# Optimization experiments

Hardware: AMD Instinct MI355X
Metric: run time of the kernel (lower is better)

Reference implementation:

```python
import jax, jax.numpy as jnp
import numpy as np

N = 8192      # num_nodes
E = 262144    # edges (before self loops)
F_IN = 256    # input_dim
H = 4         # nheads
C = 32        # nhid (per-head out channels)
D = H * C     # concat dim = 128
NEG_SLOPE = 0.2
EPS = 1e-5


def setup_inputs() -> dict:
    key = jax.random.key(0)
    ks = jax.random.split(key, 12)
    s = 0.05
    x = jax.random.normal(ks[0], (N, F_IN), jnp.float32)
    adj = jax.random.randint(ks[1], (2, E), 0, N, dtype=jnp.int32)
    Wgat = jax.random.normal(ks[2], (F_IN, D), jnp.float32) * s   # GATConv lin weight
    att_src = jax.random.normal(ks[3], (H, C), jnp.float32) * s
    att_dst = jax.random.normal(ks[4], (H, C), jnp.float32) * s
    bias_gat = jax.random.normal(ks[5], (D,), jnp.float32) * s
    Wq = jax.random.normal(ks[6], (H, D, C), jnp.float32) * s     # per-head selfattention query proj
    Wk = jax.random.normal(ks[7], (H, D, C), jnp.float32) * s     # per-head selfattention key proj
    Wpro = jax.random.normal(ks[8], (D, D), jnp.float32) * s      # prolayer (no bias)
    ln_g = jnp.ones((D,), jnp.float32)
    ln_b = jnp.zeros((D,), jnp.float32)
    return {"x": x, "adj": adj, "Wgat": Wgat, "att_src": att_src,
            "att_dst": att_dst, "bias_gat": bias_gat, "Wq": Wq, "Wk": Wk,
            "Wpro": Wpro, "ln_g": ln_g, "ln_b": ln_b}


def _gat_conv(x, src, dst, Wgat, att_src, att_dst, bias_gat):
    # PyG GATConv, concat=True, add_self_loops handled by caller.
    xw = (x @ Wgat).reshape(N, H, C)                       # [N,H,C]
    a_src = jnp.einsum('nhc,hc->nh', xw, att_src)          # [N,H]
    a_dst = jnp.einsum('nhc,hc->nh', xw, att_dst)
    e = jax.nn.leaky_relu(a_src[src] + a_dst[dst], NEG_SLOPE)  # [Etot,H]
    # segment softmax over incoming edges of each destination node
    m = jax.ops.segment_max(e, dst, num_segments=N)        # [N,H]
    e = jnp.exp(e - m[dst])
    denom = jax.ops.segment_sum(e, dst, num_segments=N)    # [N,H]
    alpha = e / denom[dst]                                 # [Etot,H]
    out = jax.ops.segment_sum(xw[src] * alpha[:, :, None], dst, num_segments=N)
    return out.reshape(N, D) + bias_gat                    # [N,D]


def reference(x, adj, Wgat, att_src, att_dst, bias_gat, Wq, Wk, Wpro, ln_g, ln_b):
    # add self loops (PyG GATConv default)
    loops = jnp.arange(N, dtype=adj.dtype)
    src = jnp.concatenate([adj[0], loops])
    dst = jnp.concatenate([adj[1], loops])

    h_cat = _gat_conv(x, src, dst, Wgat, att_src, att_dst, bias_gat)  # [N,D]
    h = h_cat @ Wpro                                                   # prolayer

    # sum over nheads independent dense node self-attention heads
    q = jnp.einsum('nd,hdc->hnc', h, Wq)                   # [H,N,C]
    k = jnp.einsum('nd,hdc->hnc', h, Wk)
    scores = jnp.einsum('hnc,hmc->hnm', q, k) / jnp.sqrt(jnp.float32(C))  # [H,N,N]
    att = jax.nn.softmax(scores, axis=-1)
    temp = jnp.einsum('hnm,md->nd', att, h)                # sum of per-head att @ h

    y = temp + h                                           # residual
    mu = jnp.mean(y, axis=-1, keepdims=True)
    var = jnp.mean(jnp.square(y - mu), axis=-1, keepdims=True)
    return (y - mu) / jnp.sqrt(var + EPS) * ln_g + ln_b
```

## Files before the change

kernel.cpp:

```cpp
#include <hip/hip_runtime.h>
#include <math.h>

#define N_NODES 8192
#define E_EDGES 262144
#define ETOT (E_EDGES + N_NODES)
#define F_IN 256
#define NH 4
#define NC 32
#define DD 128
#define NEG_SLOPE 0.2f
#define LN_EPS 1e-5f
#define QK_SCALE (1.4426950408889634f / 5.656854249492381f)

typedef __attribute__((ext_vector_type(8))) short bf16x8;
typedef __attribute__((ext_vector_type(4))) float f32x4;

__device__ __forceinline__ float fexp2(float x) { return __builtin_amdgcn_exp2f(x); }
__device__ __forceinline__ float flog2(float x) { return __builtin_amdgcn_logf(x); }
__device__ __forceinline__ float frcp(float x)  { return __builtin_amdgcn_rcpf(x); }

__device__ __forceinline__ unsigned short f2bf(float f) {
    unsigned u = __float_as_uint(f);
    u += 0x7FFFu + ((u >> 16) & 1u);
    return (unsigned short)(u >> 16);
}
__device__ __forceinline__ unsigned pk2bf(float lo, float hi) {
    unsigned a = __float_as_uint(lo) + 0x8000u;
    unsigned b = __float_as_uint(hi) + 0x8000u;
    return __builtin_amdgcn_perm(b, a, 0x07060302u);
}

__global__ __launch_bounds__(256) void k_cvt(const float* __restrict__ Wgat,
                                             const float* __restrict__ Wpro,
                                             const float* __restrict__ Wq,
                                             const float* __restrict__ Wk,
                                             unsigned short* __restrict__ Wgt,
                                             unsigned short* __restrict__ Wpt,
                                             unsigned short* __restrict__ Wqt,
                                             unsigned short* __restrict__ Wkt) {
    int t = blockIdx.x * 256 + threadIdx.x;
    if (t < 32768) {
        int c = t >> 8, k = t & 255;
        Wgt[t] = f2bf(Wgat[(size_t)k * 128 + c]);
    } else if (t < 49152) {
        int i = t - 32768, c = i >> 7, k = i & 127;
        Wpt[i] = f2bf(Wpro[(size_t)k * 128 + c]);
    } else if (t < 65536) {
        int i = t - 49152, h = i >> 12, r = i & 4095, c = r >> 7, k = r & 127;
        Wqt[i] = f2bf(Wq[h * 4096 + k * 32 + c]);
    } else if (t < 81920) {
        int i = t - 65536, h = i >> 12, r = i & 4095, c = r >> 7, k = r & 127;
        Wkt[i] = f2bf(Wk[h * 4096 + k * 32 + c]);
    }
}

__global__ __launch_bounds__(256) void k_gemm_att(const float* __restrict__ x,
                                                  const unsigned short* __restrict__ Wgt,
                                                  const float* __restrict__ att_src,
                                                  const float* __restrict__ att_dst,
                                                  float* __restrict__ xw,
                                                  float* __restrict__ asrc,
                                                  float* __restrict__ adst) {
    __shared__ unsigned short xs[32 * 256];
    const int tid = threadIdx.x;
    const int w = tid >> 6, lane = tid & 63, lq = lane & 15, g = lane >> 4;
    const int n0 = blockIdx.x * 32;
#pragma unroll
    for (int m = 0; m < 4; ++m) {
        int lin = m * 256 + tid;
        int row = lin >> 5, ch = lin & 31;
        const float* src = &x[(size_t)(n0 + row) * 256 + ch * 8];
        float4 v0 = *(const float4*)src;
        float4 v1 = *(const float4*)(src + 4);
        uint4 o;
        o.x = (unsigned)f2bf(v0.x) | ((unsigned)f2bf(v0.y) << 16);
        o.y = (unsigned)f2bf(v0.z) | ((unsigned)f2bf(v0.w) << 16);
        o.z = (unsigned)f2bf(v1.x) | ((unsigned)f2bf(v1.y) << 16);
        o.w = (unsigned)f2bf(v1.z) | ((unsigned)f2bf(v1.w) << 16);
        *(uint4*)&xs[row * 256 + ((ch + row) & 31) * 8] = o;
    }
    __syncthreads();
    f32x4 zero = {0.f, 0.f, 0.f, 0.f};
    f32x4 acc[2][2];
#pragma unroll
    for (int s = 0; s < 2; ++s) { acc[s][0] = zero; acc[s][1] = zero; }
#pragma unroll
    for (int kb = 0; kb < 8; ++kb) {
        bf16x8 af[2], bf[2];
#pragma unroll
        for (int s = 0; s < 2; ++s) {
            int row = s * 16 + lq;
            af[s] = *(const bf16x8*)&xs[row * 256 + (((kb * 4 + g) + row) & 31) * 8];
        }
#pragma unroll
        for (int c = 0; c < 2; ++c)
            bf[c] = *(const bf16x8*)(Wgt + (size_t)(w * 32 + c * 16 + lq) * 256 + kb * 32 + g * 8);
#pragma unroll
        for (int s = 0; s < 2; ++s)
#pragma unroll
            for (int c = 0; c < 2; ++c)
                acc[s][c] = __builtin_amdgcn_mfma_f32_16x16x32_bf16(af[s], bf[c], acc[s][c], 0, 0, 0);
    }
#pragma unroll
    for (int s = 0; s < 2; ++s)
#pragma unroll
        for (int c = 0; c < 2; ++c)
#pragma unroll
            for (int r = 0; r < 4; ++r)
                xw[(size_t)(n0 + s * 16 + 4 * g + r) * DD + w * 32 + c * 16 + lq] = acc[s][c][r];
    float avs0 = att_src[w * 32 + lq],      avd0 = att_dst[w * 32 + lq];
    float avs1 = att_src[w * 32 + 16 + lq], avd1 = att_dst[w * 32 + 16 + lq];
#pragma unroll
    for (int s = 0; s < 2; ++s) {
        f32x4 vs, vd;
#pragma unroll
        for (int r = 0; r < 4; ++r) {
            vs[r] = acc[s][0][r] * avs0 + acc[s][1][r] * avs1;
            vd[r] = acc[s][0][r] * avd0 + acc[s][1][r] * avd1;
        }
#pragma unroll
        for (int off = 1; off < 16; off <<= 1)
#pragma unroll
            for (int r = 0; r < 4; ++r) {
                vs[r] += __shfl_xor(vs[r], off);
                vd[r] += __shfl_xor(vd[r], off);
            }
        if (lq == 0) {
#pragma unroll
            for (int r = 0; r < 4; ++r) {
                asrc[(n0 + s * 16 + 4 * g + r) * 4 + w] = vs[r];
                adst[(n0 + s * 16 + 4 * g + r) * 4 + w] = vd[r];
            }
        }
    }
}

__global__ __launch_bounds__(256) void k_gemm_pro(const float* __restrict__ hcat,
                                                  const unsigned short* __restrict__ Wpt,
                                                  const unsigned short* __restrict__ Wqt,
                                                  const unsigned short* __restrict__ Wkt,
                                                  float* __restrict__ hbuf,
                                                  unsigned short* __restrict__ Htb,
                                                  unsigned short* __restrict__ Qb,
                                                  unsigned short* __restrict__ Kb) {
    __shared__ unsigned short xs[32 * 128];
    __shared__ unsigned short hsd[32 * 128];
    const int tid = threadIdx.x;
    const int w = tid >> 6, lane = tid & 63, lq = lane & 15, g = lane >> 4;
    const int n0 = blockIdx.x * 32;
#pragma unroll
    for (int m = 0; m < 2; ++m) {
        int lin = m * 256 + tid;
        int row = lin >> 4, ch = lin & 15;
        const float* src = &hcat[(size_t)(n0 + row) * 128 + ch * 8];
        float4 v0 = *(const float4*)src;
        float4 v1 = *(const float4*)(src + 4);
        uint4 o;
        o.x = (unsigned)f2bf(v0.x) | ((unsigned)f2bf(v0.y) << 16);
        o.y = (unsigned)f2bf(v0.z) | ((unsigned)f2bf(v0.w) << 16);
        o.z = (unsigned)f2bf(v1.x) | ((unsigned)f2bf(v1.y) << 16);
        o.w = (unsigned)f2bf(v1.z) | ((unsigned)f2bf(v1.w) << 16);
        *(uint4*)&xs[row * 128 + ((ch + row) & 15) * 8] = o;
    }
    __syncthreads();
    f32x4 zero = {0.f, 0.f, 0.f, 0.f};
    f32x4 acc[2][2];
#pragma unroll
    for (int s = 0; s < 2; ++s) { acc[s][0] = zero; acc[s][1] = zero; }
#pragma unroll
    for (int kb = 0; kb < 4; ++kb) {
        bf16x8 af[2], bf[2];
#pragma unroll
        for (int s = 0; s < 2; ++s) {
            int row = s * 16 + lq;
            af[s] = *(const bf16x8*)&xs[row * 128 + (((kb * 4 + g) + row) & 15) * 8];
        }
#pragma unroll
        for (int c = 0; c < 2; ++c)
            bf[c] = *(const bf16x8*)(Wpt + (size_t)(w * 32 + c * 16 + lq) * 128 + kb * 32 + g * 8);
#pragma unroll
        for (int s = 0; s < 2; ++s)
#pragma unroll
            for (int c = 0; c < 2; ++c)
                acc[s][c] = __builtin_amdgcn_mfma_f32_16x16x32_bf16(af[s], bf[c], acc[s][c], 0, 0, 0);
    }
#pragma unroll
    for (int s = 0; s < 2; ++s)
#pragma unroll
        for (int c = 0; c < 2; ++c) {
            int col = w * 32 + c * 16 + lq;
#pragma unroll
            for (int r = 0; r < 4; ++r) {
                int row = s * 16 + 4 * g + r;
                hbuf[(size_t)(n0 + row) * 128 + col] = acc[s][c][r];
                hsd[row * 128 + (((col >> 3) + row) & 15) * 8 + (col & 7)] = f2bf(acc[s][c][r]);
            }
            uint2 hp;
            hp.x = pk2bf(acc[s][c][0], acc[s][c][1]);
            hp.y = pk2bf(acc[s][c][2], acc[s][c][3]);
            *(uint2*)(Htb + (size_t)col * N_NODES + n0 + s * 16 + 4 * g) = hp;
        }
    __syncthreads();
    f32x4 aq[2][2], ak[2][2];
#pragma unroll
    for (int s = 0; s < 2; ++s)
#pragma unroll
        for (int c = 0; c < 2; ++c) { aq[s][c] = zero; ak[s][c] = zero; }
#pragma unroll
    for (int kb = 0; kb < 4; ++kb) {
        bf16x8 af[2], bq[2], bk[2];
#pragma unroll
        for (int s = 0; s < 2; ++s) {
            int row = s * 16 + lq;
            af[s] = *(const bf16x8*)&hsd[row * 128 + (((kb * 4 + g) + row) & 15) * 8];
        }
#pragma unroll
        for (int c = 0; c < 2; ++c) {
            size_t widx = ((size_t)w * 32 + c * 16 + lq) * 128 + kb * 32 + g * 8;
            bq[c] = *(const bf16x8*)(Wqt + widx);
            bk[c] = *(const bf16x8*)(Wkt + widx);
        }
#pragma unroll
        for (int s = 0; s < 2; ++s)
#pragma unroll
            for (int c = 0; c < 2; ++c) {
                aq[s][c] = __builtin_amdgcn_mfma_f32_16x16x32_bf16(af[s], bq[c], aq[s][c], 0, 0, 0);
                ak[s][c] = __builtin_amdgcn_mfma_f32_16x16x32_bf16(af[s], bk[c], ak[s][c], 0, 0, 0);
            }
    }
#pragma unroll
    for (int s = 0; s < 2; ++s)
#pragma unroll
        for (int c = 0; c < 2; ++c)
#pragma unroll
            for (int r = 0; r < 4; ++r) {
                size_t nidx = (size_t)w * N_NODES + n0 + s * 16 + 4 * g + r;
                Qb[nidx * NC + c * 16 + lq] = f2bf(aq[s][c][r] * QK_SCALE);
                Kb[nidx * NC + c * 16 + lq] = f2bf(ak[s][c][r]);
            }
}

__device__ __forceinline__ void edge_sd(int e, const int* adj, int& s, int& d) {
    if (e < E_EDGES) { s = adj[e]; d = adj[E_EDGES + e]; }
    else { s = e - E_EDGES; d = s; }
}

__global__ void k_deg(const int* __restrict__ adj, int* __restrict__ deg) {
    int e = blockIdx.x * blockDim.x + threadIdx.x;
    if (e >= ETOT) return;
    int d = (e < E_EDGES) ? adj[E_EDGES + e] : e - E_EDGES;
    atomicAdd(&deg[d], 1);
}

__global__ __launch_bounds__(1024) void k_scan(const int* __restrict__ deg,
                                               int* __restrict__ rowptr,
                                               int* __restrict__ cursor) {
    __shared__ int sm[1024];
    int t = threadIdx.x;
    int v[8], sum = 0;
#pragma unroll
    for (int j = 0; j < 8; ++j) { v[j] = deg[t * 8 + j]; sum += v[j]; }
    sm[t] = sum;
    __syncthreads();
    for (int off = 1; off < 1024; off <<= 1) {
        int x = (t >= off) ? sm[t - off] : 0;
        __syncthreads();
        sm[t] += x;
        __syncthreads();
    }
    int base = sm[t] - sum;
#pragma unroll
    for (int j = 0; j < 8; ++j) {
        rowptr[t * 8 + j] = base;
        cursor[t * 8 + j] = base;
        base += v[j];
    }
    if (t == 1023) rowptr[8192] = base;
}

__global__ void k_fill(const int* __restrict__ adj, const float* __restrict__ asrc,
                       const float* __restrict__ adst, int* __restrict__ cursor,
                       int* __restrict__ src_csr, float* __restrict__ p_csr,
                       float* __restrict__ nodesum) {
    int e = blockIdx.x * blockDim.x + threadIdx.x;
    if (e >= ETOT) return;
    int s, d; edge_sd(e, adj, s, d);
    int pos = atomicAdd(&cursor[d], 1);
    float4 as4 = *(const float4*)&asrc[s * 4];
    float4 ad4 = *(const float4*)&adst[d * 4];
    const float L2E = 1.4426950408889634f;
    float v;
    float4 p;
    v = as4.x + ad4.x; v = v > 0.f ? v : NEG_SLOPE * v; p.x = fexp2(v * L2E);
    v = as4.y + ad4.y; v = v > 0.f ? v : NEG_SLOPE * v; p.y = fexp2(v * L2E);
    v = as4.z + ad4.z; v = v > 0.f ? v : NEG_SLOPE * v; p.z = fexp2(v * L2E);
    v = as4.w + ad4.w; v = v > 0.f ? v : NEG_SLOPE * v; p.w = fexp2(v * L2E);
    src_csr[pos] = s;
    *(float4*)&p_csr[(size_t)pos * 4] = p;
    atomicAdd(&nodesum[d * 4 + 0], p.x);
    atomicAdd(&nodesum[d * 4 + 1], p.y);
    atomicAdd(&nodesum[d * 4 + 2], p.z);
    atomicAdd(&nodesum[d * 4 + 3], p.w);
}

__global__ __launch_bounds__(256) void k_aggregate(const int* __restrict__ rowptr,
                                                   const int* __restrict__ src_csr,
                                                   const float* __restrict__ p_csr,
                                                   const float* __restrict__ nodesum,
                                                   const float* __restrict__ xw,
                                                   const float* __restrict__ bias,
                                                   float* __restrict__ hcat) {
    int n = blockIdx.x * 2 + (threadIdx.x >> 7);
    int c = threadIdx.x & 127;
    int h = c >> 5;
    int beg = rowptr[n], end = rowptr[n + 1];
    float rden = frcp(nodesum[n * 4 + h]);
    float acc = bias[c];
    int i = beg;
    for (; i + 4 <= end; i += 4) {
        int s0 = src_csr[i], s1 = src_csr[i + 1], s2 = src_csr[i + 2], s3 = src_csr[i + 3];
        float a0 = p_csr[(size_t)i * 4 + h];
        float a1 = p_csr[(size_t)(i + 1) * 4 + h];
        float a2 = p_csr[(size_t)(i + 2) * 4 + h];
        float a3 = p_csr[(size_t)(i + 3) * 4 + h];
        acc += a0 * xw[(size_t)s0 * DD + c] + a1 * xw[(size_t)s1 * DD + c]
             + a2 * xw[(size_t)s2 * DD + c] + a3 * xw[(size_t)s3 * DD + c];
    }
    for (; i < end; ++i) {
        int s0 = src_csr[i];
        acc += p_csr[(size_t)i * 4 + h] * xw[(size_t)s0 * DD + c];
    }
    float norm = acc - bias[c];
    hcat[(size_t)n * DD + c] = bias[c] + norm * rden;
}

__global__ __launch_bounds__(256) void k_attn_l(const unsigned short* __restrict__ Qb,
                                                const unsigned short* __restrict__ Kb,
                                                float* __restrict__ lsum) {
    const int tid = threadIdx.x;
    const int w = tid >> 6;
    const int lane = tid & 63;
    const int lq = lane & 15;
    const int g = lane >> 4;
    const int q0 = blockIdx.x * 64;
    const int ks = blockIdx.y;
    f32x4 zero = {0.f, 0.f, 0.f, 0.f};

    bf16x8 qf[4];
#pragma unroll
    for (int j = 0; j < 4; ++j)
        qf[j] = *(const bf16x8*)(Qb + ((size_t)w * N_NODES + q0 + j * 16 + lq) * NC + g * 8);
    const unsigned short* Kp = Kb + (size_t)w * N_NODES * NC;

    float l[4] = {0.f, 0.f, 0.f, 0.f};
    for (int kt = 0; kt < 16; ++kt) {
        const int k0 = ks * 1024 + kt * 64;
#pragma unroll
        for (int t = 0; t < 4; ++t) {
            const bf16x8 kf = *(const bf16x8*)(Kp + (size_t)(k0 + t * 16 + lq) * NC + g * 8);
#pragma unroll
            for (int j = 0; j < 4; ++j) {
                f32x4 st = __builtin_amdgcn_mfma_f32_16x16x32_bf16(kf, qf[j], zero, 0, 0, 0);
                l[j] += (fexp2(st[0]) + fexp2(st[1])) + (fexp2(st[2]) + fexp2(st[3]));
            }
        }
    }
#pragma unroll
    for (int j = 0; j < 4; ++j) {
        float lj = l[j];
        lj += __shfl_xor(lj, 16); lj += __shfl_xor(lj, 32);
        if (lane < 16) atomicAdd(&lsum[w * N_NODES + q0 + j * 16 + lq], lj);
    }
}

__global__ __launch_bounds__(256, 2) void k_attn_pv(
        const unsigned short* __restrict__ Qb,
        const unsigned short* __restrict__ Kb,
        const unsigned short* __restrict__ Htb,
        const float* __restrict__ lsum,
        float* __restrict__ Opart) {
    __shared__ unsigned short htl[128 * 64];
    __shared__ unsigned short plds[32 * 64];
    const int tid = threadIdx.x;
    const int w = tid >> 6;
    const int lane = tid & 63;
    const int lq = lane & 15;
    const int g = lane >> 4;
    const int q0 = blockIdx.x * 32;
    const int ks = blockIdx.y;
    const int sd = tid >> 3, sc = tid & 7;
    f32x4 zero = {0.f, 0.f, 0.f, 0.f};

    float lg0[4], lg1[4];
    bf16x8 qreg0[4], qreg1[4];
#pragma unroll
    for (int h = 0; h < 4; ++h) {
        lg0[h] = -flog2(lsum[h * N_NODES + q0 + lq]);
        lg1[h] = -flog2(lsum[h * N_NODES + q0 + 16 + lq]);
        qreg0[h] = *(const bf16x8*)(Qb + ((size_t)h * N_NODES + q0 + lq) * NC + g * 8);
        qreg1[h] = *(const bf16x8*)(Qb + ((size_t)h * N_NODES + q0 + 16 + lq) * NC + g * 8);
    }

    f32x4 acc[2][2];
#pragma unroll
    for (int a = 0; a < 2; ++a) { acc[a][0] = zero; acc[a][1] = zero; }

    const int wch = 2 * w + (g >> 1);
    const int whalf = (g & 1) * 8;

    for (int kt = 0; kt < 16; ++kt) {
        const int k0 = ks * 1024 + kt * 64;
        __syncthreads();
#pragma unroll
        for (int mm = 0; mm < 4; ++mm) {
            int d = mm * 32 + sd;
            uint4 v = *(const uint4*)(Htb + (size_t)d * N_NODES + k0 + sc * 8);
            *(uint4*)&htl[d * 64 + ((sc + d) & 7) * 8] = v;
        }
        f32x4 ps0 = zero, ps1 = zero;
#pragma unroll
        for (int h = 0; h < 4; ++h) {
            const bf16x8 kf = *(const bf16x8*)(Kb + ((size_t)h * N_NODES + k0 + w * 16 + lq) * NC + g * 8);
            f32x4 st0 = __builtin_amdgcn_mfma_f32_16x16x32_bf16(kf, qreg0[h], zero, 0, 0, 0);
            f32x4 st1 = __builtin_amdgcn_mfma_f32_16x16x32_bf16(kf, qreg1[h], zero, 0, 0, 0);
#pragma unroll
            for (int r = 0; r < 4; ++r) {
                ps0[r] += fexp2(st0[r] + lg0[h]);
                ps1[r] += fexp2(st1[r] + lg1[h]);
            }
        }
        uint2 pk;
        pk.x = pk2bf(ps0[0], ps0[1]); pk.y = pk2bf(ps0[2], ps0[3]);
        {
            int row = lq;
            *(uint2*)((char*)plds + row * 128 + ((wch + row) & 7) * 16 + whalf) = pk;
        }
        pk.x = pk2bf(ps1[0], ps1[1]); pk.y = pk2bf(ps1[2], ps1[3]);
        {
            int row = 16 + lq;
            *(uint2*)((char*)plds + row * 128 + ((wch + row) & 7) * 16 + whalf) = pk;
        }
        __syncthreads();
#pragma unroll
        for (int kc = 0; kc < 2; ++kc) {
            int row0 = lq, row1 = 16 + lq;
            const bf16x8 af0 = *(const bf16x8*)((char*)plds + row0 * 128 + ((kc * 4 + g + row0) & 7) * 16);
            const bf16x8 af1 = *(const bf16x8*)((char*)plds + row1 * 128 + ((kc * 4 + g + row1) & 7) * 16);
#pragma unroll
            for (int dl = 0; dl < 2; ++dl) {
                int dd = (w * 2 + dl) * 16 + lq;
                const bf16x8 bf = *(const bf16x8*)&htl[dd * 64 + ((kc * 4 + g + dd) & 7) * 8];
                acc[dl][0] = __builtin_amdgcn_mfma_f32_16x16x32_bf16(af0, bf, acc[dl][0], 0, 0, 0);
                acc[dl][1] = __builtin_amdgcn_mfma_f32_16x16x32_bf16(af1, bf, acc[dl][1], 0, 0, 0);
            }
        }
    }
    const size_t ob = (size_t)ks * N_NODES + q0;
#pragma unroll
    for (int dl = 0; dl < 2; ++dl) {
        int d = (w * 2 + dl) * 16 + lq;
#pragma unroll
        for (int s = 0; s < 2; ++s)
#pragma unroll
            for (int r = 0; r < 4; ++r)
                Opart[(ob + s * 16 + 4 * g + r) * DD + d] = acc[dl][s][r];
    }
}

__global__ __launch_bounds__(128) void k_finalize(const float* __restrict__ Opart,
                                                  const float* __restrict__ hb,
                                                  const float* __restrict__ g,
                                                  const float* __restrict__ b,
                                                  float* __restrict__ out) {
    __shared__ float red[2];
    int n = blockIdx.x, c = threadIdx.x;
    const size_t ND = (size_t)N_NODES * DD;
    size_t idx = (size_t)n * DD + c;
    float y = hb[idx];
#pragma unroll
    for (int i = 0; i < 8; ++i) y += Opart[i * ND + idx];
    float s = y;
#pragma unroll
    for (int off = 1; off < 64; off <<= 1) s += __shfl_xor(s, off);
    if ((c & 63) == 0) red[c >> 6] = s;
    __syncthreads();
    float mu = (red[0] + red[1]) * (1.f / 128.f);
    float dv = y - mu;
    float vs = dv * dv;
#pragma unroll
    for (int off = 1; off < 64; off <<= 1) vs += __shfl_xor(vs, off);
    __syncthreads();
    if ((c & 63) == 0) red[c >> 6] = vs;
    __syncthreads();
    float rstd = rsqrtf((red[0] + red[1]) * (1.f / 128.f) + LN_EPS);
    out[idx] = dv * rstd * g[c] + b[c];
}

extern "C" void kernel_launch(void* const* d_in, const int* in_sizes, int n_in,
                              void* d_out, int out_size, void* d_ws, size_t ws_size,
                              hipStream_t stream) {
    const float* x        = (const float*)d_in[0];
    const int*   adj      = (const int*)d_in[1];
    const float* Wgat     = (const float*)d_in[2];
    const float* att_src  = (const float*)d_in[3];
    const float* att_dst  = (const float*)d_in[4];
    const float* bias_gat = (const float*)d_in[5];
    const float* Wq       = (const float*)d_in[6];
    const float* Wk       = (const float*)d_in[7];
    const float* Wpro     = (const float*)d_in[8];
    const float* ln_g     = (const float*)d_in[9];
    const float* ln_b     = (const float*)d_in[10];
    float* out = (float*)d_out;

    const size_t ND = (size_t)N_NODES * DD;
    unsigned short* Qb  = (unsigned short*)d_ws;
    unsigned short* Kb  = Qb + (1 << 20);
    unsigned short* Htb = Kb + (1 << 20);
    unsigned short* Wgt = Htb + (1 << 20);
    unsigned short* Wpt = Wgt + 32768;
    unsigned short* Wqt = Wpt + 16384;
    unsigned short* Wkt = Wqt + 16384;
    float* xw      = (float*)(Wkt + 16384);
    float* hcat    = xw + ND;
    float* hbuf    = hcat + ND;
    float* asrc    = hbuf + ND;
    float* adst    = asrc + N_NODES * NH;
    float* nodesum = adst + N_NODES * NH;
    float* lsum    = nodesum + N_NODES * NH;
    int*   deg     = (int*)(lsum + N_NODES * NH);
    int*   rowptr  = deg + 8192;
    int*   cursor  = rowptr + 8704;
    int*   src_csr = cursor + 8704;
    float* p_csr   = (float*)(src_csr + ETOT);
    float* Opart   = p_csr + (size_t)ETOT * 4;

    hipMemsetAsync(nodesum, 0, 2 * N_NODES * NH * sizeof(float), stream);
    hipMemsetAsync(deg, 0, N_NODES * sizeof(int), stream);
    k_cvt<<<320, 256, 0, stream>>>(Wgat, Wpro, Wq, Wk, Wgt, Wpt, Wqt, Wkt);
    k_gemm_att<<<N_NODES / 32, 256, 0, stream>>>(x, Wgt, att_src, att_dst, xw, asrc, adst);
    int eblocks = (ETOT + 255) / 256;
    k_deg<<<eblocks, 256, 0, stream>>>(adj, deg);
    k_scan<<<1, 1024, 0, stream>>>(deg, rowptr, cursor);
    k_fill<<<eblocks, 256, 0, stream>>>(adj, asrc, adst, cursor, src_csr, p_csr, nodesum);
    k_aggregate<<<N_NODES / 2, 256, 0, stream>>>(rowptr, src_csr, p_csr, nodesum, xw, bias_gat, hcat);
    k_gemm_pro<<<N_NODES / 32, 256, 0, stream>>>(hcat, Wpt, Wqt, Wkt, hbuf, Htb, Qb, Kb);
    dim3 lgrid(N_NODES / 64, 8);
    k_attn_l<<<lgrid, 256, 0, stream>>>(Qb, Kb, lsum);
    dim3 agrid(N_NODES / 32, 8);
    k_attn_pv<<<agrid, 256, 0, stream>>>(Qb, Kb, Htb, lsum, Opart);
    k_finalize<<<N_NODES, 128, 0, stream>>>(Opart, hbuf, ln_g, ln_b, out);
}
```

Measured before the change: 319.3 us.

## Pack edge index and bf16 weights into one CSR record, drop atomic denominators

The edge fill kernel now writes one 16-byte record per edge holding the source index and the four per-head exponentiated scores packed as bf16. It no longer does four float atomicAdds per edge into a per-node denominator. The aggregation kernel reads these records, takes its head's weight, and computes the softmax denominator itself as it accumulates. This removes a large volume of contended atomics and one memset, and merges two gathers into one. The cost is bf16 rounding of the attention weights; the rounding is consistent between numerator and denominator.

Result: faster. 266.0 us (-16.7%).

```diff
diff --git a/kernel.cpp b/kernel.cpp
--- a/kernel.cpp
+++ b/kernel.cpp
@@ -280,8 +280,7 @@
 
 __global__ void k_fill(const int* __restrict__ adj, const float* __restrict__ asrc,
                        const float* __restrict__ adst, int* __restrict__ cursor,
-                       int* __restrict__ src_csr, float* __restrict__ p_csr,
-                       float* __restrict__ nodesum) {
+                       uint4* __restrict__ rec_csr) {
     int e = blockIdx.x * blockDim.x + threadIdx.x;
     if (e >= ETOT) return;
     int s, d; edge_sd(e, adj, s, d);
@@ -295,18 +294,16 @@
     v = as4.y + ad4.y; v = v > 0.f ? v : NEG_SLOPE * v; p.y = fexp2(v * L2E);
     v = as4.z + ad4.z; v = v > 0.f ? v : NEG_SLOPE * v; p.z = fexp2(v * L2E);
     v = as4.w + ad4.w; v = v > 0.f ? v : NEG_SLOPE * v; p.w = fexp2(v * L2E);
-    src_csr[pos] = s;
-    *(float4*)&p_csr[(size_t)pos * 4] = p;
-    atomicAdd(&nodesum[d * 4 + 0], p.x);
-    atomicAdd(&nodesum[d * 4 + 1], p.y);
-    atomicAdd(&nodesum[d * 4 + 2], p.z);
-    atomicAdd(&nodesum[d * 4 + 3], p.w);
+    uint4 rec;
+    rec.x = (unsigned)s;
+    rec.y = pk2bf(p.x, p.y);
+    rec.z = pk2bf(p.z, p.w);
+    rec.w = 0u;
+    rec_csr[pos] = rec;
 }
 
 __global__ __launch_bounds__(256) void k_aggregate(const int* __restrict__ rowptr,
-                                                   const int* __restrict__ src_csr,
-                                                   const float* __restrict__ p_csr,
-                                                   const float* __restrict__ nodesum,
+                                                   const uint4* __restrict__ rec_csr,
                                                    const float* __restrict__ xw,
                                                    const float* __restrict__ bias,
                                                    float* __restrict__ hcat) {
@@ -314,24 +311,25 @@
     int c = threadIdx.x & 127;
     int h = c >> 5;
     int beg = rowptr[n], end = rowptr[n + 1];
-    float rden = frcp(nodesum[n * 4 + h]);
-    float acc = bias[c];
+    float acc = 0.f, den = 0.f;
     int i = beg;
-    for (; i + 4 <= end; i += 4) {
-        int s0 = src_csr[i], s1 = src_csr[i + 1], s2 = src_csr[i + 2], s3 = src_csr[i + 3];
-        float a0 = p_csr[(size_t)i * 4 + h];
-        float a1 = p_csr[(size_t)(i + 1) * 4 + h];
-        float a2 = p_csr[(size_t)(i + 2) * 4 + h];
-        float a3 = p_csr[(size_t)(i + 3) * 4 + h];
-        acc += a0 * xw[(size_t)s0 * DD + c] + a1 * xw[(size_t)s1 * DD + c]
-             + a2 * xw[(size_t)s2 * DD + c] + a3 * xw[(size_t)s3 * DD + c];
-    }
-    for (; i < end; ++i) {
-        int s0 = src_csr[i];
-        acc += p_csr[(size_t)i * 4 + h] * xw[(size_t)s0 * DD + c];
-    }
-    float norm = acc - bias[c];
-    hcat[(size_t)n * DD + c] = bias[c] + norm * rden;
+    for (; i + 2 <= end; i += 2) {
+        uint4 r0 = rec_csr[i], r1 = rec_csr[i + 1];
+        unsigned w0 = (h < 2) ? r0.y : r0.z;
+        unsigned w1 = (h < 2) ? r1.y : r1.z;
+        float p0 = __uint_as_float((h & 1) ? (w0 & 0xFFFF0000u) : (w0 << 16));
+        float p1 = __uint_as_float((h & 1) ? (w1 & 0xFFFF0000u) : (w1 << 16));
+        den += p0 + p1;
+        acc += p0 * xw[(size_t)r0.x * DD + c] + p1 * xw[(size_t)r1.x * DD + c];
+    }
+    if (i < end) {
+        uint4 r0 = rec_csr[i];
+        unsigned w0 = (h < 2) ? r0.y : r0.z;
+        float p0 = __uint_as_float((h & 1) ? (w0 & 0xFFFF0000u) : (w0 << 16));
+        den += p0;
+        acc += p0 * xw[(size_t)r0.x * DD + c];
+    }
+    hcat[(size_t)n * DD + c] = bias[c] + acc * frcp(den);
 }
 
 __global__ __launch_bounds__(256) void k_attn_l(const unsigned short* __restrict__ Qb,
@@ -525,24 +523,21 @@
     float* hbuf    = hcat + ND;
     float* asrc    = hbuf + ND;
     float* adst    = asrc + N_NODES * NH;
-    float* nodesum = adst + N_NODES * NH;
-    float* lsum    = nodesum + N_NODES * NH;
+    float* lsum    = adst + N_NODES * NH;
     int*   deg     = (int*)(lsum + N_NODES * NH);
     int*   rowptr  = deg + 8192;
     int*   cursor  = rowptr + 8704;
-    int*   src_csr = cursor + 8704;
-    float* p_csr   = (float*)(src_csr + ETOT);
-    float* Opart   = p_csr + (size_t)ETOT * 4;
-
-    hipMemsetAsync(nodesum, 0, 2 * N_NODES * NH * sizeof(float), stream);
-    hipMemsetAsync(deg, 0, N_NODES * sizeof(int), stream);
+    uint4* rec_csr = (uint4*)(cursor + 8704);
+    float* Opart   = (float*)(rec_csr + ETOT);
+
+    hipMemsetAsync(lsum, 0, N_NODES * NH * sizeof(float) + N_NODES * sizeof(int), stream);
     k_cvt<<<320, 256, 0, stream>>>(Wgat, Wpro, Wq, Wk, Wgt, Wpt, Wqt, Wkt);
     k_gemm_att<<<N_NODES / 32, 256, 0, stream>>>(x, Wgt, att_src, att_dst, xw, asrc, adst);
     int eblocks = (ETOT + 255) / 256;
     k_deg<<<eblocks, 256, 0, stream>>>(adj, deg);
     k_scan<<<1, 1024, 0, stream>>>(deg, rowptr, cursor);
-    k_fill<<<eblocks, 256, 0, stream>>>(adj, asrc, adst, cursor, src_csr, p_csr, nodesum);
-    k_aggregate<<<N_NODES / 2, 256, 0, stream>>>(rowptr, src_csr, p_csr, nodesum, xw, bias_gat, hcat);
+    k_fill<<<eblocks, 256, 0, stream>>>(adj, asrc, adst, cursor, rec_csr);
+    k_aggregate<<<N_NODES / 2, 256, 0, stream>>>(rowptr, rec_csr, xw, bias_gat, hcat);
     k_gemm_pro<<<N_NODES / 32, 256, 0, stream>>>(hcat, Wpt, Wqt, Wkt, hbuf, Htb, Qb, Kb);
     dim3 lgrid(N_NODES / 64, 8);
     k_attn_l<<<lgrid, 256, 0, stream>>>(Qb, Kb, lsum);
```
